# Kernel optimization log

Measured on AMD Instinct MI355X. Metric: run time of the kernel, lower is better.

Reference implementation:

```python
import jax, jax.numpy as jnp
import numpy as np

N_NODES = 100000
N_EDGES = 600000
D = 128
NUM_RELS = 200


def setup_inputs() -> dict:
    key = jax.random.key(0)
    ks = jax.random.split(key, 12)
    s = 1.0 / np.sqrt(D)
    return {
        "h": jax.random.normal(ks[0], (N_NODES, D), jnp.float32),
        "prev_h": jax.random.normal(ks[1], (N_NODES, D), jnp.float32),
        "emb_rel": jax.random.normal(ks[2], (NUM_RELS, D), jnp.float32),
        "norm": jax.random.uniform(ks[3], (N_NODES, 1), jnp.float32),
        "weight_neighbor": jax.random.normal(ks[4], (D, D), jnp.float32) * s,
        "loop_weight": jax.random.normal(ks[5], (D, D), jnp.float32) * s,
        "evolve_loop_weight": jax.random.normal(ks[6], (D, D), jnp.float32) * s,
        "skip_connect_weight": jax.random.normal(ks[7], (D, D), jnp.float32) * s,
        "skip_connect_bias": jnp.zeros((D,), jnp.float32),
        "src": jax.random.randint(ks[8], (N_EDGES,), 0, N_NODES, jnp.int64),
        "dst": jax.random.randint(ks[9], (N_EDGES,), 0, N_NODES, jnp.int64),
        "etype": jax.random.randint(ks[10], (N_EDGES,), 0, NUM_RELS, jnp.int64),
    }


def reference(h, prev_h, emb_rel, norm, weight_neighbor, loop_weight,
              evolve_loop_weight, skip_connect_weight, skip_connect_bias,
              src, dst, etype):
    n = h.shape[0]
    # self-loop message: nodes with in-degree > 0 use loop_weight, else evolve_loop_weight
    in_deg = jax.ops.segment_sum(jnp.ones_like(dst, dtype=jnp.float32), dst,
                                 num_segments=n)  # [N]
    loop_message = jnp.where(in_deg[:, None] > 0,
                             h @ loop_weight,
                             h @ evolve_loop_weight)  # [N, D]
    # skip gate from previous layer hidden state
    skip_weight = jax.nn.sigmoid(prev_h @ skip_connect_weight + skip_connect_bias)
    # msg_func: gather src node feats + relation embedding, per-edge GEMM
    msg = (h[src] + emb_rel[etype]) @ weight_neighbor  # [E, D]
    # fn.sum scatter aggregation, then apply_func: multiply by node norm
    agg = jax.ops.segment_sum(msg, dst, num_segments=n)  # [N, D]
    node_repr = agg * norm
    # skip_connect (prev_h non-empty) + self_loop branch
    node_repr = node_repr + loop_message
    node_repr = skip_weight * node_repr + (1.0 - skip_weight) * prev_h
    # activation
    return jax.nn.relu(node_repr)
```

## Files before the change

kernel.cpp:

```cpp
#include <hip/hip_runtime.h>

#define DD 128
#define SCHUNK 4096

typedef __attribute__((ext_vector_type(8))) short short8;
typedef __attribute__((ext_vector_type(4))) float f32x4;
typedef __attribute__((ext_vector_type(2))) float f32x2;
typedef __attribute__((ext_vector_type(4))) int i32x4;
typedef __attribute__((ext_vector_type(4))) unsigned int u32x4;

__device__ __forceinline__ unsigned short f2bf(float f) {
    union { float f; unsigned int i; } c; c.f = f;
    unsigned int x = c.i;
    return (unsigned short)((x + 0x7fffu + ((x >> 16) & 1u)) >> 16);
}
__device__ __forceinline__ float bfu(unsigned short u) {
    union { unsigned int i; float f; } c; c.i = ((unsigned int)u) << 16; return c.f;
}
__device__ __forceinline__ f32x2 bf2lohi(unsigned int w) {
    union { unsigned int i; float f; } lo, hi;
    lo.i = w << 16;
    hi.i = w & 0xFFFF0000u;
    return (f32x2){lo.f, hi.f};
}
__device__ __forceinline__ void gload_lds16(const void* g, void* l) {
    __builtin_amdgcn_global_load_lds(
        (const __attribute__((address_space(1))) unsigned int*)g,
        (__attribute__((address_space(3))) unsigned int*)l, 16, 0, 0);
}
__device__ __forceinline__ int idx_at(const int* p, int e, int is64) {
    return is64 ? p[2 * e] : p[e];
}
__device__ __forceinline__ int block_is64(const int* dst, int nE, int* s_flag) {
    if (threadIdx.x == 0) *s_flag = 0;
    __syncthreads();
    int w = 2 * (int)threadIdx.x + 1;
    if (threadIdx.x < 128 && w < nE && dst[w] != 0) atomicOr(s_flag, 1);
    __syncthreads();
    return !*s_flag;
}

__global__ __launch_bounds__(256) void prep_k(
    const float* __restrict__ h,
    const float* __restrict__ W0, const float* __restrict__ W1,
    const float* __restrict__ W2, const float* __restrict__ emb,
    const int* __restrict__ dst,
    unsigned short* __restrict__ hB,
    unsigned short* __restrict__ embB, unsigned short* __restrict__ Wt,
    int* __restrict__ deg, int nN, int nEmbEl, int nE) {
    int tid = threadIdx.x;
    int bid = blockIdx.x;
    int nHistB = (nE + 1023) / 1024;
    if (bid < nHistB) {
        __shared__ int s_flag;
        int is64 = block_is64(dst, nE, &s_flag);
        int e0 = bid * 1024 + tid * 4;
        #pragma unroll
        for (int j = 0; j < 4; ++j) {
            int e = e0 + j;
            if (e < nE) atomicAdd(deg + idx_at(dst, e, is64), 1);
        }
        return;
    }
    bid -= nHistB;
    int totalH = nN * DD;
    int nConvH = (totalH + 8191) / 8192;
    if (bid < nConvH) {
        int base0 = bid * 8192;
        if (base0 + 8192 <= totalH) {
            int base = base0 + tid * 8;
            f32x4 x[4][2];
            #pragma unroll
            for (int i = 0; i < 4; ++i) {
                x[i][0] = *(const f32x4*)(h + base + i * 2048);
                x[i][1] = *(const f32x4*)(h + base + i * 2048 + 4);
            }
            #pragma unroll
            for (int i = 0; i < 4; ++i) {
                short8 p;
                #pragma unroll
                for (int j = 0; j < 4; ++j) {
                    p[j]     = (short)f2bf(x[i][0][j]);
                    p[4 + j] = (short)f2bf(x[i][1][j]);
                }
                *(short8*)(hB + base + i * 2048) = p;
            }
        } else {
            #pragma unroll
            for (int i = 0; i < 4; ++i) {
                int b2 = base0 + i * 2048 + tid * 8;
                if (b2 + 8 <= totalH) {
                    f32x4 x0 = *(const f32x4*)(h + b2);
                    f32x4 x1 = *(const f32x4*)(h + b2 + 4);
                    short8 p;
                    #pragma unroll
                    for (int j = 0; j < 4; ++j) {
                        p[j]     = (short)f2bf(x0[j]);
                        p[4 + j] = (short)f2bf(x1[j]);
                    }
                    *(short8*)(hB + b2) = p;
                } else {
                    for (int j = b2; j < totalH && j < b2 + 8; ++j)
                        hB[j] = f2bf(h[j]);
                }
            }
        }
        return;
    }
    bid -= nConvH;
    if (bid < 48) {
        const float* Ws[3] = {W0, W1, W2};
        int w = bid >> 4, chunk = bid & 15;
        unsigned short* T = Wt + w * (DD * DD);
        #pragma unroll
        for (int i = 0; i < 4; ++i) {
            int t = chunk * 1024 + i * 256 + tid;
            int n = t >> 7, k = t & 127;
            T[t] = f2bf(Ws[w][k * DD + n]);
        }
        return;
    }
    bid -= 48;
    int base = bid * 2048 + tid * 8;
    if (base + 8 <= nEmbEl) {
        f32x4 x0 = *(const f32x4*)(emb + base);
        f32x4 x1 = *(const f32x4*)(emb + base + 4);
        short8 p;
        #pragma unroll
        for (int j = 0; j < 4; ++j) {
            p[j]     = (short)f2bf(x0[j]);
            p[4 + j] = (short)f2bf(x1[j]);
        }
        *(short8*)(embB + base) = p;
    } else {
        for (int j = base; j < nEmbEl; ++j) embB[j] = f2bf(emb[j]);
    }
}

__global__ __launch_bounds__(1024) void scan1_k(const int* deg, int* off, int* bsum,
                                                int nN) {
    __shared__ int s[1024];
    int t = threadIdx.x, i = blockIdx.x * 1024 + t;
    int v = (i < nN) ? deg[i] : 0;
    s[t] = v;
    __syncthreads();
    for (int d = 1; d < 1024; d <<= 1) {
        int x = (t >= d) ? s[t - d] : 0;
        __syncthreads();
        s[t] += x;
        __syncthreads();
    }
    if (i < nN) off[i] = s[t] - v;
    if (t == 1023) bsum[blockIdx.x] = s[1023];
}

__global__ __launch_bounds__(1024) void scan23_k(const int* bsum, int* off,
                                                 int* cursorB, int nN, int nB) {
    __shared__ int s[1024];
    int t = threadIdx.x;
    s[t] = (t < nB) ? bsum[t] : 0;
    __syncthreads();
    for (int d = 1; d < 1024; d <<= 1) {
        int x = (t >= d) ? s[t - d] : 0;
        __syncthreads();
        s[t] += x;
        __syncthreads();
    }
    int base = (blockIdx.x == 0) ? 0 : s[blockIdx.x - 1];
    int i = blockIdx.x * 1024 + t;
    if (i < nN) {
        int o = off[i] + base;
        off[i] = o;
        if ((i & 127) == 0) cursorB[i >> 7] = o;
    }
}

__global__ __launch_bounds__(256) void sort1_k(
    const int* __restrict__ src, const int* __restrict__ dst,
    const int* __restrict__ et, int nE, int nBuck,
    int* __restrict__ cursorB, unsigned int* __restrict__ staging) {
    __shared__ int hist[2048];
    __shared__ int rbase[2048];
    __shared__ unsigned short ranks[SCHUNK];
    __shared__ int s_flag;
    int tid = threadIdx.x;
    int is64 = block_is64(dst, nE, &s_flag);
    for (int i = tid; i < nBuck; i += 256) hist[i] = 0;
    __syncthreads();
    int cbase = blockIdx.x * SCHUNK;
    #pragma unroll
    for (int j = 0; j < SCHUNK / 256; ++j) {
        int e = cbase + j * 256 + tid;
        if (e < nE) {
            int d = idx_at(dst, e, is64);
            ranks[j * 256 + tid] = (unsigned short)atomicAdd(&hist[d >> 7], 1);
        }
    }
    __syncthreads();
    for (int b = tid; b < nBuck; b += 256) {
        int c = hist[b];
        if (c) rbase[b] = atomicAdd(cursorB + b, c);
    }
    __syncthreads();
    #pragma unroll
    for (int j = 0; j < SCHUNK / 256; ++j) {
        int e = cbase + j * 256 + tid;
        if (e < nE) {
            int d = idx_at(dst, e, is64);
            unsigned int wd = (unsigned int)idx_at(src, e, is64) |
                              ((unsigned int)idx_at(et, e, is64) << 17) |
                              ((unsigned int)(d & 127) << 25);
            staging[rbase[d >> 7] + (int)ranks[j * 256 + tid]] = wd;
        }
    }
}

__global__ __launch_bounds__(256) void sort2_k(
    const unsigned int* __restrict__ staging, const int* __restrict__ off,
    int nN, int nE, unsigned int* __restrict__ edges) {
    __shared__ int cur[128];
    int b = blockIdx.x;
    int first = b << 7;
    int tid = threadIdx.x;
    if (tid < 128 && first + tid < nN) cur[tid] = off[first + tid];
    int rStart = off[first];
    int nxt = first + 128;
    int rEnd = (nxt < nN) ? off[nxt] : nE;
    __syncthreads();
    for (int i = rStart + tid; i < rEnd; i += 256) {
        unsigned int wd = staging[i];
        int p = atomicAdd(&cur[wd >> 25], 1);
        edges[p] = wd & 0x1FFFFFFu;
    }
}

__global__ __launch_bounds__(256) void gather_k(
    const unsigned short* __restrict__ hB, const unsigned short* __restrict__ embB,
    const unsigned int* __restrict__ edges, const int* __restrict__ off,
    const int* __restrict__ deg, const float* __restrict__ normv,
    char* __restrict__ aggP, int nN) {
    int lane = threadIdx.x & 63;
    int l16 = lane & 15;
    int v = blockIdx.x * 16 + ((threadIdx.x >> 6) << 2) + (lane >> 4);
    if (v >= nN) return;
    int b = off[v], n = deg[v];
    f32x2 a2[4] = {{0.f, 0.f}, {0.f, 0.f}, {0.f, 0.f}, {0.f, 0.f}};
    for (int m = 0; m < n; m += 2) {
        bool e1 = (m + 1) < n;
        unsigned int w0 = edges[b + m];
        unsigned int w1 = e1 ? edges[b + m + 1] : 0u;
        short8 h0 = *(const short8*)(hB + (size_t)(w0 & 0x1FFFFu) * DD + l16 * 8);
        short8 r0 = *(const short8*)(embB + (size_t)(w0 >> 17) * DD + l16 * 8);
        short8 h1, r1;
        if (e1) {
            h1 = *(const short8*)(hB + (size_t)(w1 & 0x1FFFFu) * DD + l16 * 8);
            r1 = *(const short8*)(embB + (size_t)(w1 >> 17) * DD + l16 * 8);
        }
        union { short8 s; u32x4 u; } ch0, cr0;
        ch0.s = h0; cr0.s = r0;
        #pragma unroll
        for (int k = 0; k < 4; ++k) {
            a2[k] += bf2lohi(ch0.u[k]);
            a2[k] += bf2lohi(cr0.u[k]);
        }
        if (e1) {
            union { short8 s; u32x4 u; } ch1, cr1;
            ch1.s = h1; cr1.s = r1;
            #pragma unroll
            for (int k = 0; k < 4; ++k) {
                a2[k] += bf2lohi(ch1.u[k]);
                a2[k] += bf2lohi(cr1.u[k]);
            }
        }
    }
    float nm = normv[v];
    unsigned int pk[4];
    #pragma unroll
    for (int k = 0; k < 4; ++k) {
        float x0 = a2[k][0] * nm, x1 = a2[k][1] * nm;
        asm("v_cvt_pk_bf16_f32 %0, %1, %2" : "=v"(pk[k]) : "v"(x0), "v"(x1));
    }
    i32x4 w;
    w[0] = (int)pk[0]; w[1] = (int)pk[1]; w[2] = (int)pk[2]; w[3] = (int)pk[3];
    *(i32x4*)(aggP + (size_t)v * 512 + l16 * 16) = w;
}

__global__ __launch_bounds__(256, 2) void fused_k(
    const unsigned short* __restrict__ hB,
    const float* __restrict__ prevh,
    const float* __restrict__ bias,
    const char* __restrict__ aggP,
    const unsigned short* __restrict__ Wt,
    float* __restrict__ out, int nN, int nTiles) {
    extern __shared__ unsigned short lds[];
    const int lane = threadIdx.x & 63;
    const int wv = threadIdx.x >> 6;
    const int q = lane >> 4, cl = lane & 15;
    const int ncb = wv * 32;
    const int stride = gridDim.x;

    int t = blockIdx.x;
    if (t >= nTiles) return;

    short8 bn[4][2], bl[4][2], bs[4][2];
    #pragma unroll
    for (int ks = 0; ks < 4; ++ks)
        #pragma unroll
        for (int nt = 0; nt < 2; ++nt) {
            int n = (ncb + nt * 16 + cl) * DD + ks * 32 + q * 8;
            bn[ks][nt] = *(const short8*)(Wt + n);
            bl[ks][nt] = *(const short8*)(Wt + DD * DD + n);
            bs[ks][nt] = *(const short8*)(Wt + 2 * DD * DD + n);
        }
    const float b0 = bias[ncb + cl], b1 = bias[ncb + 16 + cl];

    const int r0 = lane >> 4;
    const int c16 = lane & 15;

    {
        int node_base = t * 32;
        #pragma unroll
        for (int it = 0; it < 2; ++it) {
            int r = it * 16 + wv * 4 + r0;
            int row = node_base + r; if (row > nN - 1) row = nN - 1;
            int sw = (c16 ^ (r & 15)) << 4;
            char* bptr = (char*)lds + (it * 16 + wv * 4) * 256;
            gload_lds16(aggP + (size_t)row * 512 + sw, bptr);
            gload_lds16((const char*)hB + (size_t)row * 256 + sw, bptr + 8192);
        }
        f32x4 p0[2], p1[2];
        #pragma unroll
        for (int it = 0; it < 2; ++it) {
            int pos = it * 512 + lane * 8;
            int node = node_base + wv * 8 + (pos >> 7);
            if (node > nN - 1) node = nN - 1;
            const float* g = prevh + (size_t)node * DD + (pos & 127);
            p0[it] = *(const f32x4*)g;
            p1[it] = *(const f32x4*)(g + 4);
        }
        #pragma unroll
        for (int it = 0; it < 2; ++it) {
            int pos = it * 512 + lane * 8;
            int r = wv * 8 + (pos >> 7);
            int c = (pos & 127) >> 3;
            short8 p;
            #pragma unroll
            for (int j = 0; j < 4; ++j) {
                p[j]     = (short)f2bf(p0[it][j]);
                p[4 + j] = (short)f2bf(p1[it][j]);
            }
            *(short8*)((char*)lds + 16384 + r * 256 + ((c ^ (r & 15)) << 4)) = p;
        }
    }
    __syncthreads();

    int cur = 0;
    for (;;) {
        int node_base = t * 32;
        int tn = t + stride;
        bool more = (tn < nTiles);

        f32x4 p0[2], p1[2];
        if (more) {
            int nb2 = tn * 32;
            char* dbuf = (char*)lds + (cur ^ 1) * 24576;
            #pragma unroll
            for (int it = 0; it < 2; ++it) {
                int r = it * 16 + wv * 4 + r0;
                int row = nb2 + r; if (row > nN - 1) row = nN - 1;
                int sw = (c16 ^ (r & 15)) << 4;
                char* bptr = dbuf + (it * 16 + wv * 4) * 256;
                gload_lds16(aggP + (size_t)row * 512 + sw, bptr);
                gload_lds16((const char*)hB + (size_t)row * 256 + sw, bptr + 8192);
            }
            #pragma unroll
            for (int it = 0; it < 2; ++it) {
                int pos = it * 512 + lane * 8;
                int node = nb2 + wv * 8 + (pos >> 7);
                if (node > nN - 1) node = nN - 1;
                const float* g = prevh + (size_t)node * DD + (pos & 127);
                p0[it] = *(const f32x4*)g;
                p1[it] = *(const f32x4*)(g + 4);
            }
        }

        const unsigned short* lA = lds + cur * 12288;
        const unsigned short* lH = lA + 4096;
        const unsigned short* lP = lA + 8192;

        f32x4 accM[2][2], accG[2][2];
        #pragma unroll
        for (int mt = 0; mt < 2; ++mt)
            #pragma unroll
            for (int nt = 0; nt < 2; ++nt) {
                accM[mt][nt] = (f32x4){0.f, 0.f, 0.f, 0.f};
                accG[mt][nt] = (f32x4){0.f, 0.f, 0.f, 0.f};
            }
        #pragma unroll
        for (int ks = 0; ks < 4; ++ks) {
            int swz = ((ks * 4 + q) ^ cl) << 3;
            #pragma unroll
            for (int mt = 0; mt < 2; ++mt) {
                int off = (mt * 16 + cl) * 128 + swz;
                short8 aA = *(const short8*)(lA + off);
                short8 aH = *(const short8*)(lH + off);
                short8 aP = *(const short8*)(lP + off);
                #pragma unroll
                for (int nt = 0; nt < 2; ++nt) {
                    accM[mt][nt] = __builtin_amdgcn_mfma_f32_16x16x32_bf16(
                        aA, bn[ks][nt], accM[mt][nt], 0, 0, 0);
                    accM[mt][nt] = __builtin_amdgcn_mfma_f32_16x16x32_bf16(
                        aH, bl[ks][nt], accM[mt][nt], 0, 0, 0);
                    accG[mt][nt] = __builtin_amdgcn_mfma_f32_16x16x32_bf16(
                        aP, bs[ks][nt], accG[mt][nt], 0, 0, 0);
                }
            }
        }

        #pragma unroll
        for (int mt = 0; mt < 2; ++mt) {
            #pragma unroll
            for (int r = 0; r < 4; ++r) {
                int nrow = mt * 16 + q * 4 + r;
                int node = node_base + nrow;
                if (node >= nN) continue;
                #pragma unroll
                for (int nt = 0; nt < 2; ++nt) {
                    int col = ncb + nt * 16 + cl;
                    float pv = bfu(lP[nrow * 128 +
                                      ((((col >> 3) ^ (nrow & 15)) << 3) | (col & 7))]);
                    float sg = 1.0f / (1.0f + __expf(-(accG[mt][nt][r] +
                                                       (nt ? b1 : b0))));
                    float o  = sg * accM[mt][nt][r] + (1.0f - sg) * pv;
                    out[(size_t)node * DD + col] = (o > 0.f ? o : 0.f);
                }
            }
        }

        if (more) {
            char* dbuf = (char*)lds + (cur ^ 1) * 24576;
            #pragma unroll
            for (int it = 0; it < 2; ++it) {
                int pos = it * 512 + lane * 8;
                int r = wv * 8 + (pos >> 7);
                int c = (pos & 127) >> 3;
                short8 p;
                #pragma unroll
                for (int j = 0; j < 4; ++j) {
                    p[j]     = (short)f2bf(p0[it][j]);
                    p[4 + j] = (short)f2bf(p1[it][j]);
                }
                *(short8*)(dbuf + 16384 + r * 256 + ((c ^ (r & 15)) << 4)) = p;
            }
        }
        __syncthreads();
        if (!more) break;
        cur ^= 1;
        t = tn;
    }
}

__global__ __launch_bounds__(256) void fix_k(
    const float* __restrict__ h, const float* __restrict__ prevh,
    const float* __restrict__ bias, const float* __restrict__ We,
    const float* __restrict__ Wsk, const int* __restrict__ deg,
    float* __restrict__ out, int nN, int chunk) {
    __shared__ int list[256];
    __shared__ int cnt;
    __shared__ float hrow[DD], prow[DD], res[2][DD];
    int tid = threadIdx.x;
    int base = blockIdx.x * chunk;
    for (int c = base; c < base + chunk && c < nN; c += 256) {
        if (tid == 0) cnt = 0;
        __syncthreads();
        int v = c + tid;
        if (v < nN && v < base + chunk && deg[v] == 0)
            list[atomicAdd(&cnt, 1)] = v;
        __syncthreads();
        int m = cnt;
        for (int i = 0; i < m; ++i) {
            int node = list[i];
            if (tid < DD) hrow[tid] = h[(size_t)node * DD + tid];
            else prow[tid - DD] = prevh[(size_t)node * DD + tid - DD];
            __syncthreads();
            int col = tid & (DD - 1);
            int half = tid >> 7;
            const float* W = half ? Wsk : We;
            const float* x = half ? prow : hrow;
            float s = 0.f;
            for (int k = 0; k < DD; ++k) s += x[k] * W[k * DD + col];
            res[half][col] = s;
            __syncthreads();
            if (tid < DD) {
                float sg = 1.0f / (1.0f + __expf(-(res[1][col] + bias[col])));
                float o  = sg * res[0][col] + (1.0f - sg) * prow[col];
                out[(size_t)node * DD + col] = (o > 0.f ? o : 0.f);
            }
            __syncthreads();
        }
        __syncthreads();
    }
}

extern "C" void kernel_launch(void* const* d_in, const int* in_sizes, int n_in,
                              void* d_out, int out_size, void* d_ws, size_t ws_size,
                              hipStream_t stream) {
    const float* h     = (const float*)d_in[0];
    const float* prevh = (const float*)d_in[1];
    const float* emb   = (const float*)d_in[2];
    const float* normv = (const float*)d_in[3];
    const float* Wn    = (const float*)d_in[4];
    const float* Wl    = (const float*)d_in[5];
    const float* We    = (const float*)d_in[6];
    const float* Wsk   = (const float*)d_in[7];
    const float* bias  = (const float*)d_in[8];
    const int* src   = (const int*)d_in[9];
    const int* dst   = (const int*)d_in[10];
    const int* etype = (const int*)d_in[11];

    int nN = in_sizes[3];
    int nE = in_sizes[9];
    int nEmbEl = in_sizes[2];

    char* w = (char*)d_ws;
    size_t o = 0;
    unsigned short* Wt = (unsigned short*)(w + o);  o += 3 * DD * DD * 2;
    unsigned short* embB = (unsigned short*)(w + o); o += ((size_t)nEmbEl * 2 + 255) & ~(size_t)255;
    int* deg     = (int*)(w + o);  o += ((size_t)nN * 4 + 15) & ~(size_t)15;
    int* offA    = (int*)(w + o);  o += ((size_t)nN * 4 + 15) & ~(size_t)15;
    int* cursorB = (int*)(w + o);  o += 8192;
    int* bsum    = (int*)(w + o);  o += 4096;
    unsigned int* edges   = (unsigned int*)(w + o); o += ((size_t)nE * 4 + 15) & ~(size_t)15;
    unsigned int* staging = (unsigned int*)(w + o); o += ((size_t)nE * 4 + 15) & ~(size_t)15;
    unsigned short* hB = (unsigned short*)(w + o);

    int totalH = nN * DD;
    int nConvH = (totalH + 8191) / 8192;
    int nEmbB  = (nEmbEl + 2047) / 2048;
    int nHistB = (nE + 1023) / 1024;
    int nB = (nN + 1023) / 1024;
    int nBuck = (nN + 127) / 128;
    int nTiles = (nN + 31) / 32;
    int fgrid2 = nTiles < 512 ? nTiles : 512;

    hipMemsetAsync(deg, 0, (size_t)nN * sizeof(int), stream);
    prep_k<<<nHistB + nConvH + 48 + nEmbB, 256, 0, stream>>>(
        h, Wn, Wl, Wsk, emb, dst, hB, embB, Wt, deg, nN, nEmbEl, nE);
    scan1_k<<<nB, 1024, 0, stream>>>(deg, offA, bsum, nN);
    scan23_k<<<nB, 1024, 0, stream>>>(bsum, offA, cursorB, nN, nB);
    sort1_k<<<(nE + SCHUNK - 1) / SCHUNK, 256, 0, stream>>>(
        src, dst, etype, nE, nBuck, cursorB, staging);
    sort2_k<<<nBuck, 256, 0, stream>>>(staging, offA, nN, nE, edges);
    gather_k<<<(nN + 15) / 16, 256, 0, stream>>>(hB, embB, edges, offA, deg, normv,
                                                 (char*)d_out, nN);
    fused_k<<<fgrid2, 256, 49152, stream>>>(hB, prevh, bias, (const char*)d_out,
                                            Wt, (float*)d_out, nN, nTiles);
    int fgrid = 256;
    int chunk = ((nN + fgrid * 256 - 1) / (fgrid * 256)) * 256;
    fix_k<<<fgrid, 256, 0, stream>>>(h, prevh, bias, We, Wsk, deg, (float*)d_out,
                                     nN, chunk);
    (void)ws_size; (void)n_in; (void)out_size;
}
```

Before: 281.3 us.

## Replace global per-node degree histogram with per-chunk bucket histograms for CSR sort

The per-edge global atomic degree histogram and the two-level node scan are replaced by per-chunk shared-memory bucket histograms written to global memory. Each bucket is then scanned across chunks, and per-node offsets and degrees are computed inside sort2 from the staged bucket contents. This drops the degree memset, the global atomics on deg, and the cursor atomics in sort1, and makes the sort deterministic. In exchange it adds a serial per-bucket scan over about 147 chunks and an extra counting pass in sort2.

```diff
diff --git a/kernel.cpp b/kernel.cpp
--- a/kernel.cpp
+++ b/kernel.cpp
@@ -47,22 +47,28 @@
     const int* __restrict__ dst,
     unsigned short* __restrict__ hB,
     unsigned short* __restrict__ embB, unsigned short* __restrict__ Wt,
-    int* __restrict__ deg, int nN, int nEmbEl, int nE) {
+    int* __restrict__ chunkHist, int nN, int nEmbEl, int nE,
+    int nBuck, int nChunk) {
     int tid = threadIdx.x;
     int bid = blockIdx.x;
-    int nHistB = (nE + 1023) / 1024;
-    if (bid < nHistB) {
+    if (bid < nChunk) {
+        __shared__ int hist[2048];
         __shared__ int s_flag;
         int is64 = block_is64(dst, nE, &s_flag);
-        int e0 = bid * 1024 + tid * 4;
-        #pragma unroll
-        for (int j = 0; j < 4; ++j) {
-            int e = e0 + j;
-            if (e < nE) atomicAdd(deg + idx_at(dst, e, is64), 1);
-        }
+        for (int i = tid; i < nBuck; i += 256) hist[i] = 0;
+        __syncthreads();
+        int cbase = bid * SCHUNK;
+        #pragma unroll
+        for (int j = 0; j < SCHUNK / 256; ++j) {
+            int e = cbase + j * 256 + tid;
+            if (e < nE) atomicAdd(&hist[idx_at(dst, e, is64) >> 7], 1);
+        }
+        __syncthreads();
+        for (int b = tid; b < nBuck; b += 256)
+            chunkHist[bid * nBuck + b] = hist[b];
         return;
     }
-    bid -= nHistB;
+    bid -= nChunk;
     int totalH = nN * DD;
     int nConvH = (totalH + 8191) / 8192;
     if (bid < nConvH) {
@@ -137,48 +143,49 @@
     }
 }
 
-__global__ __launch_bounds__(1024) void scan1_k(const int* deg, int* off, int* bsum,
-                                                int nN) {
-    __shared__ int s[1024];
-    int t = threadIdx.x, i = blockIdx.x * 1024 + t;
-    int v = (i < nN) ? deg[i] : 0;
-    s[t] = v;
-    __syncthreads();
-    for (int d = 1; d < 1024; d <<= 1) {
-        int x = (t >= d) ? s[t - d] : 0;
-        __syncthreads();
-        s[t] += x;
-        __syncthreads();
-    }
-    if (i < nN) off[i] = s[t] - v;
-    if (t == 1023) bsum[blockIdx.x] = s[1023];
-}
-
-__global__ __launch_bounds__(1024) void scan23_k(const int* bsum, int* off,
-                                                 int* cursorB, int nN, int nB) {
-    __shared__ int s[1024];
+__global__ __launch_bounds__(256) void scanB1_k(int* __restrict__ chunkHist,
+                                                int* __restrict__ bucketTot,
+                                                int nBuck, int nChunk) {
+    int b = blockIdx.x * 256 + threadIdx.x;
+    if (b >= nBuck) return;
+    int tot = 0;
+    for (int c = 0; c < nChunk; ++c) {
+        int v = chunkHist[c * nBuck + b];
+        chunkHist[c * nBuck + b] = tot;
+        tot += v;
+    }
+    bucketTot[b] = tot;
+}
+
+__global__ __launch_bounds__(1024) void scanB2_k(const int* __restrict__ bucketTot,
+                                                 int* __restrict__ bucketBase,
+                                                 int nBuck, int nE) {
+    __shared__ int s[2048];
     int t = threadIdx.x;
-    s[t] = (t < nB) ? bsum[t] : 0;
-    __syncthreads();
-    for (int d = 1; d < 1024; d <<= 1) {
-        int x = (t >= d) ? s[t - d] : 0;
-        __syncthreads();
-        s[t] += x;
-        __syncthreads();
-    }
-    int base = (blockIdx.x == 0) ? 0 : s[blockIdx.x - 1];
-    int i = blockIdx.x * 1024 + t;
-    if (i < nN) {
-        int o = off[i] + base;
-        off[i] = o;
-        if ((i & 127) == 0) cursorB[i >> 7] = o;
-    }
+    int b0 = t, b1 = t + 1024;
+    int v0 = (b0 < nBuck) ? bucketTot[b0] : 0;
+    int v1 = (b1 < nBuck) ? bucketTot[b1] : 0;
+    s[b0] = v0;
+    s[b1] = v1;
+    __syncthreads();
+    for (int d = 1; d < 2048; d <<= 1) {
+        int x0 = (b0 >= d) ? s[b0 - d] : 0;
+        int x1 = (b1 >= d) ? s[b1 - d] : 0;
+        __syncthreads();
+        s[b0] += x0;
+        s[b1] += x1;
+        __syncthreads();
+    }
+    if (b0 < nBuck) bucketBase[b0] = s[b0] - v0;
+    if (b1 < nBuck) bucketBase[b1] = s[b1] - v1;
+    if (t == 0) bucketBase[nBuck] = nE;
 }
 
 __global__ __launch_bounds__(256) void sort1_k(
     const int* __restrict__ src, const int* __restrict__ dst,
     const int* __restrict__ et, int nE, int nBuck,
-    int* __restrict__ cursorB, unsigned int* __restrict__ staging) {
+    const int* __restrict__ chunkHist, const int* __restrict__ bucketBase,
+    unsigned int* __restrict__ staging) {
     __shared__ int hist[2048];
     __shared__ int rbase[2048];
     __shared__ unsigned short ranks[SCHUNK];
@@ -187,7 +194,8 @@
     int is64 = block_is64(dst, nE, &s_flag);
     for (int i = tid; i < nBuck; i += 256) hist[i] = 0;
     __syncthreads();
-    int cbase = blockIdx.x * SCHUNK;
+    int c = blockIdx.x;
+    int cbase = c * SCHUNK;
     #pragma unroll
     for (int j = 0; j < SCHUNK / 256; ++j) {
         int e = cbase + j * 256 + tid;
@@ -197,10 +205,8 @@
         }
     }
     __syncthreads();
-    for (int b = tid; b < nBuck; b += 256) {
-        int c = hist[b];
-        if (c) rbase[b] = atomicAdd(cursorB + b, c);
-    }
+    for (int b = tid; b < nBuck; b += 256)
+        rbase[b] = bucketBase[b] + chunkHist[c * nBuck + b];
     __syncthreads();
     #pragma unroll
     for (int j = 0; j < SCHUNK / 256; ++j) {
@@ -216,16 +222,37 @@
 }
 
 __global__ __launch_bounds__(256) void sort2_k(
-    const unsigned int* __restrict__ staging, const int* __restrict__ off,
-    int nN, int nE, unsigned int* __restrict__ edges) {
+    const unsigned int* __restrict__ staging, const int* __restrict__ bucketBase,
+    int nN, unsigned int* __restrict__ edges,
+    int* __restrict__ off, int* __restrict__ deg) {
+    __shared__ int cnt[128];
+    __shared__ int sc[128];
     __shared__ int cur[128];
     int b = blockIdx.x;
     int first = b << 7;
     int tid = threadIdx.x;
-    if (tid < 128 && first + tid < nN) cur[tid] = off[first + tid];
-    int rStart = off[first];
-    int nxt = first + 128;
-    int rEnd = (nxt < nN) ? off[nxt] : nE;
+    if (tid < 128) cnt[tid] = 0;
+    int rStart = bucketBase[b];
+    int rEnd = bucketBase[b + 1];
+    __syncthreads();
+    for (int i = rStart + tid; i < rEnd; i += 256)
+        atomicAdd(&cnt[staging[i] >> 25], 1);
+    __syncthreads();
+    if (tid < 128) sc[tid] = cnt[tid];
+    __syncthreads();
+    for (int d = 1; d < 128; d <<= 1) {
+        int x = 0;
+        if (tid < 128 && tid >= d) x = sc[tid - d];
+        __syncthreads();
+        if (tid < 128) sc[tid] += x;
+        __syncthreads();
+    }
+    if (tid < 128) {
+        int o = rStart + sc[tid] - cnt[tid];
+        cur[tid] = o;
+        int v = first + tid;
+        if (v < nN) { off[v] = o; deg[v] = cnt[tid]; }
+    }
     __syncthreads();
     for (int i = rStart + tid; i < rEnd; i += 256) {
         unsigned int wd = staging[i];
@@ -522,14 +549,18 @@
     int nE = in_sizes[9];
     int nEmbEl = in_sizes[2];
 
+    int nBuck  = (nN + 127) / 128;
+    int nChunk = (nE + SCHUNK - 1) / SCHUNK;
+
     char* w = (char*)d_ws;
     size_t o = 0;
     unsigned short* Wt = (unsigned short*)(w + o);  o += 3 * DD * DD * 2;
     unsigned short* embB = (unsigned short*)(w + o); o += ((size_t)nEmbEl * 2 + 255) & ~(size_t)255;
-    int* deg     = (int*)(w + o);  o += ((size_t)nN * 4 + 15) & ~(size_t)15;
-    int* offA    = (int*)(w + o);  o += ((size_t)nN * 4 + 15) & ~(size_t)15;
-    int* cursorB = (int*)(w + o);  o += 8192;
-    int* bsum    = (int*)(w + o);  o += 4096;
+    int* deg        = (int*)(w + o);  o += ((size_t)nN * 4 + 15) & ~(size_t)15;
+    int* offA       = (int*)(w + o);  o += ((size_t)nN * 4 + 15) & ~(size_t)15;
+    int* bucketBase = (int*)(w + o);  o += ((size_t)(nBuck + 1) * 4 + 15) & ~(size_t)15;
+    int* bucketTot  = (int*)(w + o);  o += ((size_t)nBuck * 4 + 15) & ~(size_t)15;
+    int* chunkHist  = (int*)(w + o);  o += ((size_t)nChunk * nBuck * 4 + 15) & ~(size_t)15;
     unsigned int* edges   = (unsigned int*)(w + o); o += ((size_t)nE * 4 + 15) & ~(size_t)15;
     unsigned int* staging = (unsigned int*)(w + o); o += ((size_t)nE * 4 + 15) & ~(size_t)15;
     unsigned short* hB = (unsigned short*)(w + o);
@@ -537,20 +568,18 @@
     int totalH = nN * DD;
     int nConvH = (totalH + 8191) / 8192;
     int nEmbB  = (nEmbEl + 2047) / 2048;
-    int nHistB = (nE + 1023) / 1024;
-    int nB = (nN + 1023) / 1024;
-    int nBuck = (nN + 127) / 128;
     int nTiles = (nN + 31) / 32;
     int fgrid2 = nTiles < 512 ? nTiles : 512;
 
-    hipMemsetAsync(deg, 0, (size_t)nN * sizeof(int), stream);
-    prep_k<<<nHistB + nConvH + 48 + nEmbB, 256, 0, stream>>>(
-        h, Wn, Wl, Wsk, emb, dst, hB, embB, Wt, deg, nN, nEmbEl, nE);
-    scan1_k<<<nB, 1024, 0, stream>>>(deg, offA, bsum, nN);
-    scan23_k<<<nB, 1024, 0, stream>>>(bsum, offA, cursorB, nN, nB);
-    sort1_k<<<(nE + SCHUNK - 1) / SCHUNK, 256, 0, stream>>>(
-        src, dst, etype, nE, nBuck, cursorB, staging);
-    sort2_k<<<nBuck, 256, 0, stream>>>(staging, offA, nN, nE, edges);
+    prep_k<<<nChunk + nConvH + 48 + nEmbB, 256, 0, stream>>>(
+        h, Wn, Wl, Wsk, emb, dst, hB, embB, Wt, chunkHist,
+        nN, nEmbEl, nE, nBuck, nChunk);
+    scanB1_k<<<(nBuck + 255) / 256, 256, 0, stream>>>(chunkHist, bucketTot,
+                                                      nBuck, nChunk);
+    scanB2_k<<<1, 1024, 0, stream>>>(bucketTot, bucketBase, nBuck, nE);
+    sort1_k<<<nChunk, 256, 0, stream>>>(src, dst, etype, nE, nBuck,
+                                        chunkHist, bucketBase, staging);
+    sort2_k<<<nBuck, 256, 0, stream>>>(staging, bucketBase, nN, edges, offA, deg);
     gather_k<<<(nN + 15) / 16, 256, 0, stream>>>(hB, embB, edges, offA, deg, normv,
                                                  (char*)d_out, nN);
     fused_k<<<fgrid2, 256, 49152, stream>>>(hB, prevh, bias, (const char*)d_out,
```

Measured after the change: 301.0 us. 1.07x slower.
